# Optimization experiments

Hardware: AMD Instinct MI355X
Metric: run time of the kernel (lower is better)

## Reference

```python
import jax, jax.numpy as jnp
import numpy as np

D_MODEL = 256
D_FFN = 1024
N_HEADS = 8
N_LEVELS = 4
N_POINTS = 4
SPATIAL = np.array([[60, 100], [30, 50], [15, 25], [8, 13]], dtype=np.int32)  # (H, W) per level


def _layer_norm(x, g, b, eps=1e-5):
    mu = jnp.mean(x, axis=-1, keepdims=True)
    var = jnp.mean(jnp.square(x - mu), axis=-1, keepdims=True)
    return (x - mu) * jax.lax.rsqrt(var + eps) * g + b


def _bilinear_sample(v_l, loc, aw, H, W):
    # v_l: (B,H,W,h,hd); loc: (B,Lq,h,p,2) normalized [0,1]; aw: (B,Lq,h,p)
    B = v_l.shape[0]
    h = v_l.shape[3]
    x = loc[..., 0] * W - 0.5  # grid_sample align_corners=False convention
    y = loc[..., 1] * H - 0.5
    x0 = jnp.floor(x)
    y0 = jnp.floor(y)
    lx = x - x0
    ly = y - y0
    x0i = x0.astype(jnp.int32)
    y0i = y0.astype(jnp.int32)
    bi = jnp.arange(B)[:, None, None, None]
    hi = jnp.arange(h)[None, None, :, None]

    def g(xi, yi):
        valid = (xi >= 0) & (xi < W) & (yi >= 0) & (yi < H)
        xc = jnp.clip(xi, 0, W - 1)
        yc = jnp.clip(yi, 0, H - 1)
        return v_l[bi, yc, xc, hi] * valid[..., None].astype(v_l.dtype)  # zero padding

    w00 = (1 - lx) * (1 - ly)
    w01 = lx * (1 - ly)
    w10 = (1 - lx) * ly
    w11 = lx * ly
    samp = (g(x0i, y0i) * w00[..., None] + g(x0i + 1, y0i) * w01[..., None]
            + g(x0i, y0i + 1) * w10[..., None] + g(x0i + 1, y0i + 1) * w11[..., None])
    # weighted sum over sampling points -> (B,Lq,h,hd)
    return jnp.einsum('blhpd,blhp->blhd', samp, aw)


def _msda(q, val, ref, W_value, b_value, W_off, b_off, W_attn, b_attn, W_out, b_out):
    # mmcv MultiScaleDeformableAttention (batch_first, identity=query, eval-mode dropout)
    B, Lq, C = q.shape
    hd = C // N_HEADS
    v = (val @ W_value + b_value).reshape(B, -1, N_HEADS, hd)
    off = (q @ W_off + b_off).reshape(B, Lq, N_HEADS, N_LEVELS, N_POINTS, 2)
    aw = jax.nn.softmax((q @ W_attn + b_attn).reshape(B, Lq, N_HEADS, N_LEVELS * N_POINTS), axis=-1)
    aw = aw.reshape(B, Lq, N_HEADS, N_LEVELS, N_POINTS)
    normalizer = jnp.asarray(SPATIAL[:, ::-1].copy(), dtype=q.dtype)  # (levels, 2) = (W, H)
    loc = ref[:, :, None, :, None, :] + off / normalizer[None, None, None, :, None, :]
    out = jnp.zeros((B, Lq, N_HEADS, hd), q.dtype)
    start = 0
    for lvl in range(N_LEVELS):
        H, W = int(SPATIAL[lvl, 0]), int(SPATIAL[lvl, 1])
        v_l = v[:, start:start + H * W].reshape(B, H, W, N_HEADS, hd)
        start += H * W
        out = out + _bilinear_sample(v_l, loc[:, :, :, lvl], aw[:, :, :, lvl], H, W)
    return q + out.reshape(B, Lq, C) @ W_out + b_out  # identity + output_proj


def setup_inputs() -> dict:
    key = jax.random.key(0)
    ks = jax.random.split(key, 16)
    bs, cams, nq = 1, 6, 6400
    l = int(SPATIAL.prod(axis=1).sum())
    s = 0.02
    inp = {
        'query': jax.random.normal(ks[0], (bs, nq, D_MODEL), jnp.float32),
        'key': jax.random.normal(ks[1], (bs, cams, l, D_MODEL), jnp.float32),
        'value': jax.random.normal(ks[2], (bs, cams, l, D_MODEL), jnp.float32),
        'reference_points_cam': jax.random.uniform(ks[3], (cams, bs, nq, N_LEVELS, 2), jnp.float32),
        'spatial_shapes': jnp.asarray(SPATIAL),
        'level_start_index': jnp.asarray(np.concatenate([[0], np.cumsum(SPATIAL.prod(axis=1))[:-1]]).astype(np.int32)),
        'bev_mask': jax.random.randint(ks[4], (cams, bs, nq, 4), 0, 2).astype(jnp.int32),
        'W_value': jax.random.normal(ks[5], (D_MODEL, D_MODEL), jnp.float32) * s,
        'b_value': jnp.zeros((D_MODEL,), jnp.float32),
        'W_off': jax.random.normal(ks[6], (D_MODEL, N_HEADS * N_LEVELS * N_POINTS * 2), jnp.float32) * s,
        'b_off': jax.random.normal(ks[7], (N_HEADS * N_LEVELS * N_POINTS * 2,), jnp.float32) * s,
        'W_attn': jax.random.normal(ks[8], (D_MODEL, N_HEADS * N_LEVELS * N_POINTS), jnp.float32) * s,
        'b_attn': jnp.zeros((N_HEADS * N_LEVELS * N_POINTS,), jnp.float32),
        'W_out': jax.random.normal(ks[9], (D_MODEL, D_MODEL), jnp.float32) * s,
        'b_out': jnp.zeros((D_MODEL,), jnp.float32),
        'ln1_g': jnp.ones((D_MODEL,), jnp.float32),
        'ln1_b': jnp.zeros((D_MODEL,), jnp.float32),
        'W1': jax.random.normal(ks[10], (D_MODEL, D_FFN), jnp.float32) * s,
        'b1': jnp.zeros((D_FFN,), jnp.float32),
        'W2': jax.random.normal(ks[11], (D_FFN, D_MODEL), jnp.float32) * s,
        'b2': jnp.zeros((D_MODEL,), jnp.float32),
        'ln2_g': jnp.ones((D_MODEL,), jnp.float32),
        'ln2_b': jnp.zeros((D_MODEL,), jnp.float32),
    }
    return inp


def reference(query, key, value, reference_points_cam, spatial_shapes, level_start_index, bev_mask,
              W_value, b_value, W_off, b_off, W_attn, b_attn, W_out, b_out,
              ln1_g, ln1_b, W1, b1, W2, b2, ln2_g, ln2_b):
    bs, nq, C = query.shape
    cams = key.shape[1]
    l = key.shape[2]
    # per-camera query visibility taken from batch element 0 (as in original)
    cam_mask = (bev_mask[:, 0].sum(-1) > 0).astype(query.dtype)  # (cams, nq)
    # rebatch via masking: equivalent to gather-to-padded since attention is per-query
    q_rb = (query[:, None] * cam_mask[None, :, :, None]).reshape(bs * cams, nq, C)
    ref_rb = (jnp.transpose(reference_points_cam, (1, 0, 2, 3, 4))
              * cam_mask[None, :, :, None, None]).reshape(bs * cams, nq, N_LEVELS, 2)
    val = value.reshape(bs * cams, l, C)
    attn = _msda(q_rb, val, ref_rb, W_value, b_value, W_off, b_off, W_attn, b_attn, W_out, b_out)
    attn = attn.reshape(bs, cams, nq, C)
    # scatter-add back (only visible camera contributions)
    slots = jnp.einsum('bknc,kn->bnc', attn, cam_mask)
    # visibility count (full bev_mask, per batch element)
    count = (bev_mask.sum(-1) > 0).astype(query.dtype)  # (cams, bs, nq)
    count = jnp.maximum(count.transpose(1, 2, 0).sum(-1), 1.0)  # (bs, nq)
    slots = slots / count[..., None]
    x = _layer_norm(slots + query, ln1_g, ln1_b)
    ffn = jax.nn.relu(x @ W1 + b1) @ W2 + b2
    return _layer_norm(x + ffn, ln2_g, ln2_b)
```

## Files before the change

### kernel.cpp

```cpp
#include <hip/hip_runtime.h>
#include <math.h>

#define NQ      6400
#define NCAMS   6
#define LTOT    7979
#define DM      256
#define DFFN    1024

typedef __attribute__((ext_vector_type(8))) short bf16x8;
typedef __attribute__((ext_vector_type(4))) float f32x4;

__device__ inline unsigned short f32_to_bf16(float f) {
    unsigned u = __float_as_uint(f);
    unsigned r = u + 0x7FFF + ((u >> 16) & 1);
    return (unsigned short)(r >> 16);
}

__global__ __launch_bounds__(256) void cvt_kernel(
    const float* __restrict__ src, unsigned short* __restrict__ dst, int n8)
{
    int i = blockIdx.x * 256 + threadIdx.x;
    if (i >= n8) return;
    const float4* s = (const float4*)src + (size_t)i * 2;
    float4 a = s[0], b = s[1];
    uint4 o;
    o.x = f32_to_bf16(a.x) | ((unsigned)f32_to_bf16(a.y) << 16);
    o.y = f32_to_bf16(a.z) | ((unsigned)f32_to_bf16(a.w) << 16);
    o.z = f32_to_bf16(b.x) | ((unsigned)f32_to_bf16(b.y) << 16);
    o.w = f32_to_bf16(b.z) | ((unsigned)f32_to_bf16(b.w) << 16);
    *(uint4*)(dst + (size_t)i * 8) = o;
}

__global__ __launch_bounds__(256) void wt_kernel(
    const float* __restrict__ Wv, const float* __restrict__ Woff,
    const float* __restrict__ Wattn, const float* __restrict__ Wout,
    const float* __restrict__ W1, const float* __restrict__ W2,
    unsigned short* __restrict__ wsT)
{
    int b = blockIdx.x;
    const float* src; int K, N, t0, dstoff;
    if (b < 64)       { src = Wv;    K = 256;  N = 256;  t0 = 0;   dstoff = 0; }
    else if (b < 128) { src = Woff;  K = 256;  N = 256;  t0 = 64;  dstoff = 65536; }
    else if (b < 160) { src = Wattn; K = 256;  N = 128;  t0 = 128; dstoff = 131072; }
    else if (b < 224) { src = Wout;  K = 256;  N = 256;  t0 = 160; dstoff = 163840; }
    else if (b < 480) { src = W1;    K = 256;  N = 1024; t0 = 224; dstoff = 229376; }
    else              { src = W2;    K = 1024; N = 256;  t0 = 480; dstoff = 491520; }
    int t = b - t0;
    int ntn = N >> 5;
    int kt = t / ntn, nt = t - kt * ntn;
    __shared__ float tile[32][33];
    int tx = threadIdx.x & 31, ty = threadIdx.x >> 5;
    #pragma unroll
    for (int i = 0; i < 4; ++i)
        tile[ty + i * 8][tx] = src[(size_t)(kt * 32 + ty + i * 8) * N + nt * 32 + tx];
    __syncthreads();
    #pragma unroll
    for (int i = 0; i < 4; ++i) {
        int nn = nt * 32 + ty + i * 8;
        wsT[dstoff + (size_t)nn * K + kt * 32 + tx] = f32_to_bf16(tile[tx][ty + i * 8]);
    }
}

__global__ __launch_bounds__(256) void gemm_v_kernel(
    const unsigned short* __restrict__ A, const unsigned short* __restrict__ BT,
    const float* __restrict__ bias, unsigned short* __restrict__ Cb, int M)
{
    const int K = 256;
    __shared__ __align__(16) unsigned short As[128][40];
    __shared__ __align__(16) unsigned short Bs[128][40];

    const int tid  = threadIdx.x;
    const int wave = tid >> 6, lane = tid & 63;
    const int wm = wave >> 1, wn = wave & 1;
    const int quad = lane >> 4, l16 = lane & 15;
    const int m0 = blockIdx.y * 128, n0 = blockIdx.x * 128;

    f32x4 acc[4][4] = {};

    for (int k0 = 0; k0 < K; k0 += 32) {
        #pragma unroll
        for (int i = 0; i < 2; ++i) {
            int idx = tid + 256 * i;
            int r = idx >> 2, kc = (idx & 3) * 8;
            int gr = m0 + r;
            uint4 d = (gr < M) ? *(const uint4*)(A + (size_t)gr * K + k0 + kc)
                               : make_uint4(0u, 0u, 0u, 0u);
            uint2* dst = (uint2*)&As[r][kc];
            dst[0] = make_uint2(d.x, d.y);
            dst[1] = make_uint2(d.z, d.w);
        }
        #pragma unroll
        for (int i = 0; i < 2; ++i) {
            int idx = tid + 256 * i;
            int r = idx >> 2, kc = (idx & 3) * 8;
            uint4 d = *(const uint4*)(BT + (size_t)(n0 + r) * K + k0 + kc);
            uint2* dst = (uint2*)&Bs[r][kc];
            dst[0] = make_uint2(d.x, d.y);
            dst[1] = make_uint2(d.z, d.w);
        }
        __syncthreads();
        bf16x8 af[4], bfr[4];
        #pragma unroll
        for (int mi = 0; mi < 4; ++mi)
            af[mi] = *(const bf16x8*)&As[wm * 64 + mi * 16 + l16][quad * 8];
        #pragma unroll
        for (int ni = 0; ni < 4; ++ni)
            bfr[ni] = *(const bf16x8*)&Bs[wn * 64 + ni * 16 + l16][quad * 8];
        #pragma unroll
        for (int mi = 0; mi < 4; ++mi)
            #pragma unroll
            for (int ni = 0; ni < 4; ++ni)
                acc[mi][ni] = __builtin_amdgcn_mfma_f32_16x16x32_bf16(
                    af[mi], bfr[ni], acc[mi][ni], 0, 0, 0);
        __syncthreads();
    }

    #pragma unroll
    for (int mi = 0; mi < 4; ++mi) {
        #pragma unroll
        for (int r = 0; r < 4; ++r) {
            int gm = m0 + wm * 64 + mi * 16 + quad * 4 + r;
            if (gm >= M) continue;
            int cam = gm / LTOT;
            int pix = gm - cam * LTOT;
            #pragma unroll
            for (int ni = 0; ni < 4; ++ni) {
                int gn = n0 + wn * 64 + ni * 16 + l16;
                int head = gn >> 5, ch = gn & 31;
                float v = acc[mi][ni][r] + bias[gn];
                Cb[(((size_t)(cam * 8 + head)) * LTOT + pix) * 32 + ch] = f32_to_bf16(v);
            }
        }
    }
}

__global__ __launch_bounds__(256) void gemm64_kernel(
    const unsigned short* __restrict__ A, const unsigned short* __restrict__ BT,
    const float* __restrict__ bias, float* __restrict__ C,
    unsigned short* __restrict__ Cb,
    int M, int N, int K, int mode)
{
    __shared__ __align__(16) unsigned short As[64][40];
    __shared__ __align__(16) unsigned short Bs[128][40];

    const int tid  = threadIdx.x;
    const int wave = tid >> 6, lane = tid & 63;
    const int wm = wave >> 1, wn = wave & 1;
    const int quad = lane >> 4, l16 = lane & 15;
    const int m0 = blockIdx.y * 64, n0 = blockIdx.x * 128;

    f32x4 acc[2][4] = {};

    for (int k0 = 0; k0 < K; k0 += 32) {
        {
            int r = tid >> 2, kc = (tid & 3) * 8;
            int gr = m0 + r;
            uint4 d = (gr < M) ? *(const uint4*)(A + (size_t)gr * K + k0 + kc)
                               : make_uint4(0u, 0u, 0u, 0u);
            uint2* dst = (uint2*)&As[r][kc];
            dst[0] = make_uint2(d.x, d.y);
            dst[1] = make_uint2(d.z, d.w);
        }
        #pragma unroll
        for (int i = 0; i < 2; ++i) {
            int idx = tid + 256 * i;
            int r = idx >> 2, kc = (idx & 3) * 8;
            uint4 d = *(const uint4*)(BT + (size_t)(n0 + r) * K + k0 + kc);
            uint2* dst = (uint2*)&Bs[r][kc];
            dst[0] = make_uint2(d.x, d.y);
            dst[1] = make_uint2(d.z, d.w);
        }
        __syncthreads();
        bf16x8 af[2], bfr[4];
        #pragma unroll
        for (int mi = 0; mi < 2; ++mi)
            af[mi] = *(const bf16x8*)&As[wm * 32 + mi * 16 + l16][quad * 8];
        #pragma unroll
        for (int ni = 0; ni < 4; ++ni)
            bfr[ni] = *(const bf16x8*)&Bs[wn * 64 + ni * 16 + l16][quad * 8];
        #pragma unroll
        for (int mi = 0; mi < 2; ++mi)
            #pragma unroll
            for (int ni = 0; ni < 4; ++ni)
                acc[mi][ni] = __builtin_amdgcn_mfma_f32_16x16x32_bf16(
                    af[mi], bfr[ni], acc[mi][ni], 0, 0, 0);
        __syncthreads();
    }

    #pragma unroll
    for (int mi = 0; mi < 2; ++mi) {
        #pragma unroll
        for (int r = 0; r < 4; ++r) {
            int gm = m0 + wm * 32 + mi * 16 + quad * 4 + r;
            if (gm >= M) continue;
            #pragma unroll
            for (int ni = 0; ni < 4; ++ni) {
                int gn = n0 + wn * 64 + ni * 16 + l16;
                float v = acc[mi][ni][r] + (bias ? bias[gn] : 0.f);
                if (mode == 1) {
                    Cb[(size_t)gm * N + gn] = f32_to_bf16(fmaxf(v, 0.f));
                } else {
                    C[(size_t)gm * N + gn] = v;
                }
            }
        }
    }
}

__global__ __launch_bounds__(256) void qproj_kernel(
    const unsigned short* __restrict__ A, const unsigned short* __restrict__ WqT,
    const float* __restrict__ b_off, const float* __restrict__ b_attn,
    float* __restrict__ qoff, float* __restrict__ qaw)
{
    const int K = 256;
    __shared__ __align__(16) unsigned short As[64][40];
    __shared__ __align__(16) unsigned short Bs[128][40];

    const int tid  = threadIdx.x;
    const int wave = tid >> 6, lane = tid & 63;
    const int wm = wave >> 1, wn = wave & 1;
    const int quad = lane >> 4, l16 = lane & 15;
    const int m0 = blockIdx.y * 64, n0 = blockIdx.x * 128;
    const int is_attn = (n0 == 256);

    f32x4 acc[2][4] = {};

    for (int k0 = 0; k0 < K; k0 += 32) {
        {
            int r = tid >> 2, kc = (tid & 3) * 8;
            uint4 d = *(const uint4*)(A + (size_t)(m0 + r) * K + k0 + kc);
            uint2* dst = (uint2*)&As[r][kc];
            dst[0] = make_uint2(d.x, d.y);
            dst[1] = make_uint2(d.z, d.w);
        }
        #pragma unroll
        for (int i = 0; i < 2; ++i) {
            int idx = tid + 256 * i;
            int r = idx >> 2, kc = (idx & 3) * 8;
            uint4 d = *(const uint4*)(WqT + (size_t)(n0 + r) * K + k0 + kc);
            uint2* dst = (uint2*)&Bs[r][kc];
            dst[0] = make_uint2(d.x, d.y);
            dst[1] = make_uint2(d.z, d.w);
        }
        __syncthreads();
        bf16x8 af[2], bfr[4];
        #pragma unroll
        for (int mi = 0; mi < 2; ++mi)
            af[mi] = *(const bf16x8*)&As[wm * 32 + mi * 16 + l16][quad * 8];
        #pragma unroll
        for (int ni = 0; ni < 4; ++ni)
            bfr[ni] = *(const bf16x8*)&Bs[wn * 64 + ni * 16 + l16][quad * 8];
        #pragma unroll
        for (int mi = 0; mi < 2; ++mi)
            #pragma unroll
            for (int ni = 0; ni < 4; ++ni)
                acc[mi][ni] = __builtin_amdgcn_mfma_f32_16x16x32_bf16(
                    af[mi], bfr[ni], acc[mi][ni], 0, 0, 0);
        __syncthreads();
    }

    if (is_attn) {
        #pragma unroll
        for (int mi = 0; mi < 2; ++mi) {
            #pragma unroll
            for (int r = 0; r < 4; ++r) {
                int gm = m0 + wm * 32 + mi * 16 + quad * 4 + r;
                #pragma unroll
                for (int ni = 0; ni < 4; ++ni) {
                    int gn = wn * 64 + ni * 16 + l16;
                    float v = acc[mi][ni][r] + b_attn[gn];
                    float mx = v;
                    #pragma unroll
                    for (int s = 1; s < 16; s <<= 1)
                        mx = fmaxf(mx, __shfl_xor(mx, s, 64));
                    float e = __expf(v - mx);
                    float sum = e;
                    #pragma unroll
                    for (int s = 1; s < 16; s <<= 1)
                        sum += __shfl_xor(sum, s, 64);
                    qaw[(size_t)gm * 128 + gn] = e / sum;
                }
            }
        }
    } else {
        #pragma unroll
        for (int mi = 0; mi < 2; ++mi) {
            #pragma unroll
            for (int r = 0; r < 4; ++r) {
                int gm = m0 + wm * 32 + mi * 16 + quad * 4 + r;
                #pragma unroll
                for (int ni = 0; ni < 4; ++ni) {
                    int gn = n0 + wn * 64 + ni * 16 + l16;
                    qoff[(size_t)gm * 256 + gn] = acc[mi][ni][r] + b_off[gn];
                }
            }
        }
    }
}

__global__ __launch_bounds__(256) void sample_kernel(
    const unsigned short* __restrict__ vb,
    const float* __restrict__ qoff,
    const float* __restrict__ aw,
    const float* __restrict__ refpts,
    const int*   __restrict__ bev_mask,
    unsigned short* __restrict__ outsum,
    float* __restrict__ visb)
{
    const int bid = blockIdx.x;
    const int h   = bid & 7;
    const int q0  = (bid >> 3) * 16;
    const int tid = threadIdx.x;
    const int sq  = tid >> 4;
    const int tup = tid & 15;
    const int lvl = tup >> 2;
    const int n_s = q0 + sq;
    const int tg  = (tid >> 2) & 3;
    const int cg  = tid & 3;

    __shared__ int2  s_tab[4][272];
    __shared__ float s_vis[NCAMS][16];
    __shared__ int   s_cnt[NCAMS];
    __shared__ int   s_nvis[16];

    if (tid < 96) {
        int cam = tid >> 4, q = tid & 15;
        const int* bm = bev_mask + ((size_t)cam * NQ + q0 + q) * 4;
        s_vis[cam][q] = ((bm[0] + bm[1] + bm[2] + bm[3]) > 0) ? 1.f : 0.f;
    }
    __syncthreads();
    if (tid < NCAMS) {
        float s = 0.f;
        #pragma unroll
        for (int q = 0; q < 16; ++q) s += s_vis[tid][q];
        s_cnt[tid] = (int)s;
    }
    if (tid >= 32 && tid < 48) {
        int q = tid - 32;
        float s = 0.f;
        #pragma unroll
        for (int cam = 0; cam < NCAMS; ++cam) s += s_vis[cam][q];
        s_nvis[q] = (int)s;
    }
    __syncthreads();

    const float my_aw = aw[(size_t)n_s * 128 + h * 16 + tup];
    const float offx  = qoff[(size_t)n_s * 256 + h * 32 + tup * 2];
    const float offy  = qoff[(size_t)n_s * 256 + h * 32 + tup * 2 + 1];
    const int Wl   = (lvl == 0) ? 100 : (lvl == 1) ? 50 : (lvl == 2) ? 25 : 13;
    const int Hl   = (lvl == 0) ? 60  : (lvl == 1) ? 30 : (lvl == 2) ? 15 : 8;
    const int base = (lvl == 0) ? 0   : (lvl == 1) ? 6000 : (lvl == 2) ? 7500 : 7875;
    const float dx = offx / (float)Wl;
    const float dy = offy / (float)Hl;
    const int tabi = sq * 17 + tup;

    float a0 = 0.f, a1 = 0.f, a2 = 0.f, a3 = 0.f;
    float a4 = 0.f, a5 = 0.f, a6 = 0.f, a7 = 0.f;

    for (int k = 0; k < NCAMS; ++k) {
        if (s_cnt[k] == 0) continue;
        {
            const size_t rbase = (((size_t)k * NQ + n_s) * 4 + lvl) * 2;
            float fx = (refpts[rbase + 0] + dx) * (float)Wl - 0.5f;
            float fy = (refpts[rbase + 1] + dy) * (float)Hl - 0.5f;
            float x0f = floorf(fx), y0f = floorf(fy);
            float lx = fx - x0f, ly = fy - y0f;
            int x0 = (int)x0f, y0 = (int)y0f;
            int x1 = x0 + 1, y1 = y0 + 1;
            float wb = my_aw * s_vis[k][sq];
            float w00 = (1.f - lx) * (1.f - ly) * wb;
            float w01 = lx * (1.f - ly) * wb;
            float w10 = (1.f - lx) * ly * wb;
            float w11 = lx * ly * wb;
            bool vx0 = (x0 >= 0) & (x0 < Wl), vx1 = (x1 >= 0) & (x1 < Wl);
            bool vy0 = (y0 >= 0) & (y0 < Hl), vy1 = (y1 >= 0) & (y1 < Hl);
            s_tab[0][tabi] = make_int2((vx0 & vy0) ? (base + y0 * Wl + x0) * 64 : 0,
                                       __float_as_int((vx0 & vy0) ? w00 : 0.f));
            s_tab[1][tabi] = make_int2((vx1 & vy0) ? (base + y0 * Wl + x1) * 64 : 0,
                                       __float_as_int((vx1 & vy0) ? w01 : 0.f));
            s_tab[2][tabi] = make_int2((vx0 & vy1) ? (base + y1 * Wl + x0) * 64 : 0,
                                       __float_as_int((vx0 & vy1) ? w10 : 0.f));
            s_tab[3][tabi] = make_int2((vx1 & vy1) ? (base + y1 * Wl + x1) * 64 : 0,
                                       __float_as_int((vx1 & vy1) ? w11 : 0.f));
        }
        __syncthreads();
        const char* vkh = (const char*)vb + (size_t)(k * 8 + h) * (LTOT * 64) + cg * 16;
        #pragma unroll
        for (int j = 0; j < 4; ++j) {
            int ti = sq * 17 + tg * 4 + j;
            #pragma unroll
            for (int corner = 0; corner < 4; ++corner) {
                int2 t = s_tab[corner][ti];
                float w = __int_as_float(t.y);
                uint4 d = *(const uint4*)(vkh + t.x);
                a0 += w * __uint_as_float(d.x << 16);
                a1 += w * __uint_as_float(d.x & 0xFFFF0000u);
                a2 += w * __uint_as_float(d.y << 16);
                a3 += w * __uint_as_float(d.y & 0xFFFF0000u);
                a4 += w * __uint_as_float(d.z << 16);
                a5 += w * __uint_as_float(d.z & 0xFFFF0000u);
                a6 += w * __uint_as_float(d.w << 16);
                a7 += w * __uint_as_float(d.w & 0xFFFF0000u);
            }
        }
        __syncthreads();
    }

    a0 += __shfl_xor(a0, 4, 64); a0 += __shfl_xor(a0, 8, 64);
    a1 += __shfl_xor(a1, 4, 64); a1 += __shfl_xor(a1, 8, 64);
    a2 += __shfl_xor(a2, 4, 64); a2 += __shfl_xor(a2, 8, 64);
    a3 += __shfl_xor(a3, 4, 64); a3 += __shfl_xor(a3, 8, 64);
    a4 += __shfl_xor(a4, 4, 64); a4 += __shfl_xor(a4, 8, 64);
    a5 += __shfl_xor(a5, 4, 64); a5 += __shfl_xor(a5, 8, 64);
    a6 += __shfl_xor(a6, 4, 64); a6 += __shfl_xor(a6, 8, 64);
    a7 += __shfl_xor(a7, 4, 64); a7 += __shfl_xor(a7, 8, 64);

    if ((tid & 12) == 0) {
        int nv = s_nvis[sq];
        float sc = 1.f / (float)(nv > 0 ? nv : 1);
        uint4 o;
        o.x = f32_to_bf16(a0 * sc) | ((unsigned)f32_to_bf16(a1 * sc) << 16);
        o.y = f32_to_bf16(a2 * sc) | ((unsigned)f32_to_bf16(a3 * sc) << 16);
        o.z = f32_to_bf16(a4 * sc) | ((unsigned)f32_to_bf16(a5 * sc) << 16);
        o.w = f32_to_bf16(a6 * sc) | ((unsigned)f32_to_bf16(a7 * sc) << 16);
        *(uint4*)(outsum + (size_t)n_s * 256 + h * 32 + cg * 8) = o;
    }
    if (h == 0 && tid < 16) visb[q0 + tid] = (s_nvis[tid] > 0) ? 1.f : 0.f;
}

__device__ inline float block_sum_256(float v, float* red)
{
    #pragma unroll
    for (int o = 32; o > 0; o >>= 1) v += __shfl_down(v, o, 64);
    int lane = threadIdx.x & 63, w = threadIdx.x >> 6;
    if (lane == 0) red[w] = v;
    __syncthreads();
    float t = red[0] + red[1] + red[2] + red[3];
    __syncthreads();
    return t;
}

__global__ __launch_bounds__(256) void ln1_kernel(
    const float* __restrict__ gin, const float* __restrict__ query,
    const float* __restrict__ visb, const float* __restrict__ b_out,
    const float* __restrict__ g, const float* __restrict__ b,
    float* __restrict__ xout, unsigned short* __restrict__ xbf)
{
    __shared__ float red[4];
    int n = blockIdx.x, j = threadIdx.x;
    float vs = visb[n];
    size_t idx = (size_t)n * 256 + j;
    float t = gin[idx] + query[idx] * (1.f + vs) + vs * b_out[j];
    float mu = block_sum_256(t, red) * (1.f / 256.f);
    float d = t - mu;
    float var = block_sum_256(d * d, red) * (1.f / 256.f);
    float res = d * rsqrtf(var + 1e-5f) * g[j] + b[j];
    xout[idx] = res;
    xbf[idx] = f32_to_bf16(res);
}

__global__ __launch_bounds__(256) void ln2_kernel(
    const float* __restrict__ x, const float* __restrict__ ffn,
    const float* __restrict__ g, const float* __restrict__ b,
    float* __restrict__ out)
{
    __shared__ float red[4];
    int n = blockIdx.x, j = threadIdx.x;
    size_t idx = (size_t)n * 256 + j;
    float t = x[idx] + ffn[idx];
    float mu = block_sum_256(t, red) * (1.f / 256.f);
    float d = t - mu;
    float var = block_sum_256(d * d, red) * (1.f / 256.f);
    out[idx] = d * rsqrtf(var + 1e-5f) * g[j] + b[j];
}

extern "C" void kernel_launch(void* const* d_in, const int* in_sizes, int n_in,
                              void* d_out, int out_size, void* d_ws, size_t ws_size,
                              hipStream_t stream)
{
    const float* query   = (const float*)d_in[0];
    const float* value   = (const float*)d_in[2];
    const float* refpts  = (const float*)d_in[3];
    const int*   bevmask = (const int*)d_in[6];
    const float* W_value = (const float*)d_in[7];
    const float* b_value = (const float*)d_in[8];
    const float* W_off   = (const float*)d_in[9];
    const float* b_off   = (const float*)d_in[10];
    const float* W_attn  = (const float*)d_in[11];
    const float* b_attn  = (const float*)d_in[12];
    const float* W_out   = (const float*)d_in[13];
    const float* b_out   = (const float*)d_in[14];
    const float* ln1_g   = (const float*)d_in[15];
    const float* ln1_b   = (const float*)d_in[16];
    const float* W1      = (const float*)d_in[17];
    const float* b1      = (const float*)d_in[18];
    const float* W2      = (const float*)d_in[19];
    const float* b2      = (const float*)d_in[20];
    const float* ln2_g   = (const float*)d_in[21];
    const float* ln2_b   = (const float*)d_in[22];
    float* out = (float*)d_out;

    char* ws = (char*)d_ws;
    unsigned short* vb       = (unsigned short*)(ws + 0);
    float*          xbuf     = (float*)(ws + 0);
    float*          ln_in    = (float*)(ws + 7000000);
    unsigned short* xbf      = (unsigned short*)(ws + 14000000);
    unsigned short* value_bf = (unsigned short*)(ws + 24600000);
    float*          qoff     = (float*)(ws + 24600000);
    float*          qaw      = (float*)(ws + 31200000);
    unsigned short* outsum   = (unsigned short*)(ws + 34500000);
    unsigned short* hbf      = (unsigned short*)(ws + 37800000);
    unsigned short* query_bf = (unsigned short*)(ws + 51000000);
    float*          ffnout   = (float*)(ws + 54300000);
    float*          visb     = (float*)(ws + 60900000);
    unsigned short* wsT      = (unsigned short*)(ws + 61000000);

    unsigned short* WvT = wsT;
    unsigned short* WqT = wsT + 65536;
    unsigned short* WoT = wsT + 163840;
    unsigned short* W1T = wsT + 229376;
    unsigned short* W2T = wsT + 491520;

    const int MV = NCAMS * LTOT;

    cvt_kernel<<<dim3((MV * 256 / 8 + 255) / 256), 256, 0, stream>>>(
        value, value_bf, MV * 256 / 8);
    cvt_kernel<<<dim3((NQ * 256 / 8 + 255) / 256), 256, 0, stream>>>(
        query, query_bf, NQ * 256 / 8);
    wt_kernel<<<dim3(736), 256, 0, stream>>>(
        W_value, W_off, W_attn, W_out, W1, W2, wsT);
    gemm_v_kernel<<<dim3(2, (MV + 127) / 128), 256, 0, stream>>>(
        value_bf, WvT, b_value, vb, MV);
    qproj_kernel<<<dim3(3, 100), 256, 0, stream>>>(
        query_bf, WqT, b_off, b_attn, qoff, qaw);
    sample_kernel<<<dim3(3200), 256, 0, stream>>>(
        vb, qoff, qaw, refpts, bevmask, outsum, visb);
    gemm64_kernel<<<dim3(2, 100), 256, 0, stream>>>(
        outsum, WoT, nullptr, ln_in, nullptr, NQ, 256, 256, 0);
    ln1_kernel<<<dim3(NQ), 256, 0, stream>>>(
        ln_in, query, visb, b_out, ln1_g, ln1_b, xbuf, xbf);
    gemm64_kernel<<<dim3(8, 100), 256, 0, stream>>>(
        xbf, W1T, b1, nullptr, hbf, NQ, DFFN, 256, 1);
    gemm64_kernel<<<dim3(2, 100), 256, 0, stream>>>(
        hbf, W2T, b2, ffnout, nullptr, NQ, 256, DFFN, 0);
    ln2_kernel<<<dim3(NQ), 256, 0, stream>>>(
        xbuf, ffnout, ln2_g, ln2_b, out);
}
```

Measured before the change: 332.2 us.

## Fuse bf16 conversion into GEMMs, fuse out-proj with LN1, split-K FFN2, double-buffer sampling

```diff
diff --git a/kernel.cpp b/kernel.cpp
--- a/kernel.cpp
+++ b/kernel.cpp
@@ -14,21 +14,6 @@
     unsigned u = __float_as_uint(f);
     unsigned r = u + 0x7FFF + ((u >> 16) & 1);
     return (unsigned short)(r >> 16);
-}
-
-__global__ __launch_bounds__(256) void cvt_kernel(
-    const float* __restrict__ src, unsigned short* __restrict__ dst, int n8)
-{
-    int i = blockIdx.x * 256 + threadIdx.x;
-    if (i >= n8) return;
-    const float4* s = (const float4*)src + (size_t)i * 2;
-    float4 a = s[0], b = s[1];
-    uint4 o;
-    o.x = f32_to_bf16(a.x) | ((unsigned)f32_to_bf16(a.y) << 16);
-    o.y = f32_to_bf16(a.z) | ((unsigned)f32_to_bf16(a.w) << 16);
-    o.z = f32_to_bf16(b.x) | ((unsigned)f32_to_bf16(b.y) << 16);
-    o.w = f32_to_bf16(b.z) | ((unsigned)f32_to_bf16(b.w) << 16);
-    *(uint4*)(dst + (size_t)i * 8) = o;
 }
 
 __global__ __launch_bounds__(256) void wt_kernel(
@@ -62,7 +47,7 @@
 }
 
 __global__ __launch_bounds__(256) void gemm_v_kernel(
-    const unsigned short* __restrict__ A, const unsigned short* __restrict__ BT,
+    const float* __restrict__ A, const unsigned short* __restrict__ BT,
     const float* __restrict__ bias, unsigned short* __restrict__ Cb, int M)
 {
     const int K = 256;
@@ -83,20 +68,23 @@
             int idx = tid + 256 * i;
             int r = idx >> 2, kc = (idx & 3) * 8;
             int gr = m0 + r;
-            uint4 d = (gr < M) ? *(const uint4*)(A + (size_t)gr * K + k0 + kc)
-                               : make_uint4(0u, 0u, 0u, 0u);
-            uint2* dst = (uint2*)&As[r][kc];
-            dst[0] = make_uint2(d.x, d.y);
-            dst[1] = make_uint2(d.z, d.w);
+            float4 f0, f1;
+            if (gr < M) {
+                f0 = *(const float4*)(A + (size_t)gr * K + k0 + kc);
+                f1 = *(const float4*)(A + (size_t)gr * K + k0 + kc + 4);
+            } else { f0 = make_float4(0,0,0,0); f1 = f0; }
+            uint4 o;
+            o.x = f32_to_bf16(f0.x) | ((unsigned)f32_to_bf16(f0.y) << 16);
+            o.y = f32_to_bf16(f0.z) | ((unsigned)f32_to_bf16(f0.w) << 16);
+            o.z = f32_to_bf16(f1.x) | ((unsigned)f32_to_bf16(f1.y) << 16);
+            o.w = f32_to_bf16(f1.z) | ((unsigned)f32_to_bf16(f1.w) << 16);
+            *(uint4*)&As[r][kc] = o;
         }
         #pragma unroll
         for (int i = 0; i < 2; ++i) {
             int idx = tid + 256 * i;
             int r = idx >> 2, kc = (idx & 3) * 8;
-            uint4 d = *(const uint4*)(BT + (size_t)(n0 + r) * K + k0 + kc);
-            uint2* dst = (uint2*)&Bs[r][kc];
-            dst[0] = make_uint2(d.x, d.y);
-            dst[1] = make_uint2(d.z, d.w);
+            *(uint4*)&Bs[r][kc] = *(const uint4*)(BT + (size_t)(n0 + r) * K + k0 + kc);
         }
         __syncthreads();
         bf16x8 af[4], bfr[4];
@@ -134,81 +122,8 @@
     }
 }
 
-__global__ __launch_bounds__(256) void gemm64_kernel(
-    const unsigned short* __restrict__ A, const unsigned short* __restrict__ BT,
-    const float* __restrict__ bias, float* __restrict__ C,
-    unsigned short* __restrict__ Cb,
-    int M, int N, int K, int mode)
-{
-    __shared__ __align__(16) unsigned short As[64][40];
-    __shared__ __align__(16) unsigned short Bs[128][40];
-
-    const int tid  = threadIdx.x;
-    const int wave = tid >> 6, lane = tid & 63;
-    const int wm = wave >> 1, wn = wave & 1;
-    const int quad = lane >> 4, l16 = lane & 15;
-    const int m0 = blockIdx.y * 64, n0 = blockIdx.x * 128;
-
-    f32x4 acc[2][4] = {};
-
-    for (int k0 = 0; k0 < K; k0 += 32) {
-        {
-            int r = tid >> 2, kc = (tid & 3) * 8;
-            int gr = m0 + r;
-            uint4 d = (gr < M) ? *(const uint4*)(A + (size_t)gr * K + k0 + kc)
-                               : make_uint4(0u, 0u, 0u, 0u);
-            uint2* dst = (uint2*)&As[r][kc];
-            dst[0] = make_uint2(d.x, d.y);
-            dst[1] = make_uint2(d.z, d.w);
-        }
-        #pragma unroll
-        for (int i = 0; i < 2; ++i) {
-            int idx = tid + 256 * i;
-            int r = idx >> 2, kc = (idx & 3) * 8;
-            uint4 d = *(const uint4*)(BT + (size_t)(n0 + r) * K + k0 + kc);
-            uint2* dst = (uint2*)&Bs[r][kc];
-            dst[0] = make_uint2(d.x, d.y);
-            dst[1] = make_uint2(d.z, d.w);
-        }
-        __syncthreads();
-        bf16x8 af[2], bfr[4];
-        #pragma unroll
-        for (int mi = 0; mi < 2; ++mi)
-            af[mi] = *(const bf16x8*)&As[wm * 32 + mi * 16 + l16][quad * 8];
-        #pragma unroll
-        for (int ni = 0; ni < 4; ++ni)
-            bfr[ni] = *(const bf16x8*)&Bs[wn * 64 + ni * 16 + l16][quad * 8];
-        #pragma unroll
-        for (int mi = 0; mi < 2; ++mi)
-            #pragma unroll
-            for (int ni = 0; ni < 4; ++ni)
-                acc[mi][ni] = __builtin_amdgcn_mfma_f32_16x16x32_bf16(
-                    af[mi], bfr[ni], acc[mi][ni], 0, 0, 0);
-        __syncthreads();
-    }
-
-    #pragma unroll
-    for (int mi = 0; mi < 2; ++mi) {
-        #pragma unroll
-        for (int r = 0; r < 4; ++r) {
-            int gm = m0 + wm * 32 + mi * 16 + quad * 4 + r;
-            if (gm >= M) continue;
-            #pragma unroll
-            for (int ni = 0; ni < 4; ++ni) {
-                int gn = n0 + wn * 64 + ni * 16 + l16;
-                float v = acc[mi][ni][r] + (bias ? bias[gn] : 0.f);
-                if (mode == 1) {
-                    Cb[(size_t)gm * N + gn] = f32_to_bf16(fmaxf(v, 0.f));
-                } else {
-                    C[(size_t)gm * N + gn] = v;
-                }
-            }
-        }
-    }
-}
-
 __global__ __launch_bounds__(256) void qproj_kernel(
-    const unsigned short* __restrict__ A, const unsigned short* __restrict__ WqT,
+    const float* __restrict__ A, const unsigned short* __restrict__ WqT,
     const float* __restrict__ b_off, const float* __restrict__ b_attn,
     float* __restrict__ qoff, float* __restrict__ qaw)
 {
@@ -228,19 +143,20 @@
     for (int k0 = 0; k0 < K; k0 += 32) {
         {
             int r = tid >> 2, kc = (tid & 3) * 8;
-            uint4 d = *(const uint4*)(A + (size_t)(m0 + r) * K + k0 + kc);
-            uint2* dst = (uint2*)&As[r][kc];
-            dst[0] = make_uint2(d.x, d.y);
-            dst[1] = make_uint2(d.z, d.w);
+            float4 f0 = *(const float4*)(A + (size_t)(m0 + r) * K + k0 + kc);
+            float4 f1 = *(const float4*)(A + (size_t)(m0 + r) * K + k0 + kc + 4);
+            uint4 o;
+            o.x = f32_to_bf16(f0.x) | ((unsigned)f32_to_bf16(f0.y) << 16);
+            o.y = f32_to_bf16(f0.z) | ((unsigned)f32_to_bf16(f0.w) << 16);
+            o.z = f32_to_bf16(f1.x) | ((unsigned)f32_to_bf16(f1.y) << 16);
+            o.w = f32_to_bf16(f1.z) | ((unsigned)f32_to_bf16(f1.w) << 16);
+            *(uint4*)&As[r][kc] = o;
         }
         #pragma unroll
         for (int i = 0; i < 2; ++i) {
             int idx = tid + 256 * i;
             int r = idx >> 2, kc = (idx & 3) * 8;
-            uint4 d = *(const uint4*)(WqT + (size_t)(n0 + r) * K + k0 + kc);
-            uint2* dst = (uint2*)&Bs[r][kc];
-            dst[0] = make_uint2(d.x, d.y);
-            dst[1] = make_uint2(d.z, d.w);
+            *(uint4*)&Bs[r][kc] = *(const uint4*)(WqT + (size_t)(n0 + r) * K + k0 + kc);
         }
         __syncthreads();
         bf16x8 af[2], bfr[4];
@@ -318,7 +234,7 @@
     const int tg  = (tid >> 2) & 3;
     const int cg  = tid & 3;
 
-    __shared__ int2  s_tab[4][272];
+    __shared__ int2  s_tab[2][4][272];
     __shared__ float s_vis[NCAMS][16];
     __shared__ int   s_cnt[NCAMS];
     __shared__ int   s_nvis[16];
@@ -354,43 +270,53 @@
     const float dy = offy / (float)Hl;
     const int tabi = sq * 17 + tup;
 
+    int vcams[NCAMS], nvc = 0;
+    #pragma unroll
+    for (int k = 0; k < NCAMS; ++k)
+        if (s_cnt[k] > 0) vcams[nvc++] = k;
+
+    auto build_tab = [&](int k, int buf) {
+        const size_t rbase = (((size_t)k * NQ + n_s) * 4 + lvl) * 2;
+        float fx = (refpts[rbase + 0] + dx) * (float)Wl - 0.5f;
+        float fy = (refpts[rbase + 1] + dy) * (float)Hl - 0.5f;
+        float x0f = floorf(fx), y0f = floorf(fy);
+        float lx = fx - x0f, ly = fy - y0f;
+        int x0 = (int)x0f, y0 = (int)y0f;
+        int x1 = x0 + 1, y1 = y0 + 1;
+        float wb = my_aw * s_vis[k][sq];
+        float w00 = (1.f - lx) * (1.f - ly) * wb;
+        float w01 = lx * (1.f - ly) * wb;
+        float w10 = (1.f - lx) * ly * wb;
+        float w11 = lx * ly * wb;
+        bool vx0 = (x0 >= 0) & (x0 < Wl), vx1 = (x1 >= 0) & (x1 < Wl);
+        bool vy0 = (y0 >= 0) & (y0 < Hl), vy1 = (y1 >= 0) & (y1 < Hl);
+        s_tab[buf][0][tabi] = make_int2((vx0 & vy0) ? (base + y0 * Wl + x0) * 64 : 0,
+                                        __float_as_int((vx0 & vy0) ? w00 : 0.f));
+        s_tab[buf][1][tabi] = make_int2((vx1 & vy0) ? (base + y0 * Wl + x1) * 64 : 0,
+                                        __float_as_int((vx1 & vy0) ? w01 : 0.f));
+        s_tab[buf][2][tabi] = make_int2((vx0 & vy1) ? (base + y1 * Wl + x0) * 64 : 0,
+                                        __float_as_int((vx0 & vy1) ? w10 : 0.f));
+        s_tab[buf][3][tabi] = make_int2((vx1 & vy1) ? (base + y1 * Wl + x1) * 64 : 0,
+                                        __float_as_int((vx1 & vy1) ? w11 : 0.f));
+    };
+
     float a0 = 0.f, a1 = 0.f, a2 = 0.f, a3 = 0.f;
     float a4 = 0.f, a5 = 0.f, a6 = 0.f, a7 = 0.f;
 
-    for (int k = 0; k < NCAMS; ++k) {
-        if (s_cnt[k] == 0) continue;
-        {
-            const size_t rbase = (((size_t)k * NQ + n_s) * 4 + lvl) * 2;
-            float fx = (refpts[rbase + 0] + dx) * (float)Wl - 0.5f;
-            float fy = (refpts[rbase + 1] + dy) * (float)Hl - 0.5f;
-            float x0f = floorf(fx), y0f = floorf(fy);
-            float lx = fx - x0f, ly = fy - y0f;
-            int x0 = (int)x0f, y0 = (int)y0f;
-            int x1 = x0 + 1, y1 = y0 + 1;
-            float wb = my_aw * s_vis[k][sq];
-            float w00 = (1.f - lx) * (1.f - ly) * wb;
-            float w01 = lx * (1.f - ly) * wb;
-            float w10 = (1.f - lx) * ly * wb;
-            float w11 = lx * ly * wb;
-            bool vx0 = (x0 >= 0) & (x0 < Wl), vx1 = (x1 >= 0) & (x1 < Wl);
-            bool vy0 = (y0 >= 0) & (y0 < Hl), vy1 = (y1 >= 0) & (y1 < Hl);
-            s_tab[0][tabi] = make_int2((vx0 & vy0) ? (base + y0 * Wl + x0) * 64 : 0,
-                                       __float_as_int((vx0 & vy0) ? w00 : 0.f));
-            s_tab[1][tabi] = make_int2((vx1 & vy0) ? (base + y0 * Wl + x1) * 64 : 0,
-                                       __float_as_int((vx1 & vy0) ? w01 : 0.f));
-            s_tab[2][tabi] = make_int2((vx0 & vy1) ? (base + y1 * Wl + x0) * 64 : 0,
-                                       __float_as_int((vx0 & vy1) ? w10 : 0.f));
-            s_tab[3][tabi] = make_int2((vx1 & vy1) ? (base + y1 * Wl + x1) * 64 : 0,
-                                       __float_as_int((vx1 & vy1) ? w11 : 0.f));
-        }
-        __syncthreads();
+    if (nvc > 0) build_tab(vcams[0], 0);
+    __syncthreads();
+
+    int pb = 0;
+    for (int i = 0; i < nvc; ++i) {
+        int k = vcams[i];
+        if (i + 1 < nvc) build_tab(vcams[i + 1], pb ^ 1);
         const char* vkh = (const char*)vb + (size_t)(k * 8 + h) * (LTOT * 64) + cg * 16;
         #pragma unroll
         for (int j = 0; j < 4; ++j) {
             int ti = sq * 17 + tg * 4 + j;
             #pragma unroll
             for (int corner = 0; corner < 4; ++corner) {
-                int2 t = s_tab[corner][ti];
+                int2 t = s_tab[pb][corner][ti];
                 float w = __int_as_float(t.y);
                 uint4 d = *(const uint4*)(vkh + t.x);
                 a0 += w * __uint_as_float(d.x << 16);
@@ -404,6 +330,7 @@
             }
         }
         __syncthreads();
+        pb ^= 1;
     }
 
     a0 += __shfl_xor(a0, 4, 64); a0 += __shfl_xor(a0, 8, 64);
@@ -428,6 +355,179 @@
     if (h == 0 && tid < 16) visb[q0 + tid] = (s_nvis[tid] > 0) ? 1.f : 0.f;
 }
 
+__global__ __launch_bounds__(256) void projln1_kernel(
+    const unsigned short* __restrict__ A, const unsigned short* __restrict__ BT,
+    const float* __restrict__ query, const float* __restrict__ visb,
+    const float* __restrict__ b_out, const float* __restrict__ g,
+    const float* __restrict__ b,
+    float* __restrict__ xout, unsigned short* __restrict__ xbf)
+{
+    const int K = 256;
+    __shared__ __align__(16) unsigned short As[32][40];
+    __shared__ __align__(16) unsigned short Bs[256][40];
+    __shared__ float sred[2][4][4][2];
+    __shared__ float ssred[2][4][4][2];
+    __shared__ float s_mu[32], s_rs[32];
+
+    const int tid  = threadIdx.x;
+    const int wave = tid >> 6, lane = tid & 63;
+    const int wm = wave >> 1, wn = wave & 1;
+    const int quad = lane >> 4, l16 = lane & 15;
+    const int m0 = blockIdx.x * 32;
+
+    f32x4 acc[8] = {};
+
+    for (int k0 = 0; k0 < K; k0 += 32) {
+        {
+            int r = tid >> 3, kc = (tid & 7) * 4;
+            *(uint2*)&As[r][kc] = *(const uint2*)(A + (size_t)(m0 + r) * K + k0 + kc);
+        }
+        {
+            const unsigned short* src = BT + (size_t)tid * K + k0;
+            uint4 d0 = *(const uint4*)(src);
+            uint4 d1 = *(const uint4*)(src + 8);
+            uint4 d2 = *(const uint4*)(src + 16);
+            uint4 d3 = *(const uint4*)(src + 24);
+            *(uint4*)&Bs[tid][0]  = d0;
+            *(uint4*)&Bs[tid][8]  = d1;
+            *(uint4*)&Bs[tid][16] = d2;
+            *(uint4*)&Bs[tid][24] = d3;
+        }
+        __syncthreads();
+        bf16x8 af = *(const bf16x8*)&As[wm * 16 + l16][quad * 8];
+        #pragma unroll
+        for (int ni = 0; ni < 8; ++ni) {
+            bf16x8 bfr = *(const bf16x8*)&Bs[wn * 128 + ni * 16 + l16][quad * 8];
+            acc[ni] = __builtin_amdgcn_mfma_f32_16x16x32_bf16(af, bfr, acc[ni], 0, 0, 0);
+        }
+        __syncthreads();
+    }
+
+    float vals[8][4];
+    #pragma unroll
+    for (int r = 0; r < 4; ++r) {
+        int gm = m0 + wm * 16 + quad * 4 + r;
+        float vs = visb[gm];
+        float s = 0.f, ss = 0.f;
+        #pragma unroll
+        for (int ni = 0; ni < 8; ++ni) {
+            int gn = wn * 128 + ni * 16 + l16;
+            float v = acc[ni][r] + vs * b_out[gn]
+                    + query[(size_t)gm * 256 + gn] * (1.f + vs);
+            vals[ni][r] = v;
+            s += v; ss += v * v;
+        }
+        #pragma unroll
+        for (int m = 1; m < 16; m <<= 1) {
+            s  += __shfl_xor(s,  m, 64);
+            ss += __shfl_xor(ss, m, 64);
+        }
+        if (l16 == 0) {
+            sred[wm][quad][r][wn]  = s;
+            ssred[wm][quad][r][wn] = ss;
+        }
+    }
+    __syncthreads();
+    if (tid < 32) {
+        int lwm = tid >> 4, lq = (tid >> 2) & 3, lr = tid & 3;
+        float s  = sred[lwm][lq][lr][0]  + sred[lwm][lq][lr][1];
+        float ss = ssred[lwm][lq][lr][0] + ssred[lwm][lq][lr][1];
+        float mu = s * (1.f / 256.f);
+        float var = ss * (1.f / 256.f) - mu * mu;
+        s_mu[tid] = mu;
+        s_rs[tid] = rsqrtf(var + 1e-5f);
+    }
+    __syncthreads();
+
+    #pragma unroll
+    for (int r = 0; r < 4; ++r) {
+        int rowl = wm * 16 + quad * 4 + r;
+        int gm = m0 + rowl;
+        float mu = s_mu[rowl], rs = s_rs[rowl];
+        #pragma unroll
+        for (int ni = 0; ni < 8; ++ni) {
+            int gn = wn * 128 + ni * 16 + l16;
+            float res = (vals[ni][r] - mu) * rs * g[gn] + b[gn];
+            xout[(size_t)gm * 256 + gn] = res;
+            xbf[(size_t)gm * 256 + gn] = f32_to_bf16(res);
+        }
+    }
+}
+
+__global__ __launch_bounds__(256) void gemm64_kernel(
+    const unsigned short* __restrict__ A, const unsigned short* __restrict__ BT,
+    const float* __restrict__ bias, float* __restrict__ C,
+    unsigned short* __restrict__ Cb,
+    int M, int N, int K, int mode)
+{
+    __shared__ __align__(16) unsigned short As[64][40];
+    __shared__ __align__(16) unsigned short Bs[128][40];
+
+    const int tid  = threadIdx.x;
+    const int wave = tid >> 6, lane = tid & 63;
+    const int wm = wave >> 1, wn = wave & 1;
+    const int quad = lane >> 4, l16 = lane & 15;
+    const int m0 = blockIdx.y * 64, n0 = blockIdx.x * 128;
+    const int nz = gridDim.z;
+    const int klen = K / nz;
+    const int kbase = blockIdx.z * klen;
+
+    f32x4 acc[2][4] = {};
+
+    for (int k0 = kbase; k0 < kbase + klen; k0 += 32) {
+        {
+            int r = tid >> 2, kc = (tid & 3) * 8;
+            int gr = m0 + r;
+            uint4 d = (gr < M) ? *(const uint4*)(A + (size_t)gr * K + k0 + kc)
+                               : make_uint4(0u, 0u, 0u, 0u);
+            *(uint4*)&As[r][kc] = d;
+        }
+        #pragma unroll
+        for (int i = 0; i < 2; ++i) {
+            int idx = tid + 256 * i;
+            int r = idx >> 2, kc = (idx & 3) * 8;
+            *(uint4*)&Bs[r][kc] = *(const uint4*)(BT + (size_t)(n0 + r) * K + k0 + kc);
+        }
+        __syncthreads();
+        bf16x8 af[2], bfr[4];
+        #pragma unroll
+        for (int mi = 0; mi < 2; ++mi)
+            af[mi] = *(const bf16x8*)&As[wm * 32 + mi * 16 + l16][quad * 8];
+        #pragma unroll
+        for (int ni = 0; ni < 4; ++ni)
+            bfr[ni] = *(const bf16x8*)&Bs[wn * 64 + ni * 16 + l16][quad * 8];
+        #pragma unroll
+        for (int mi = 0; mi < 2; ++mi)
+            #pragma unroll
+            for (int ni = 0; ni < 4; ++ni)
+                acc[mi][ni] = __builtin_amdgcn_mfma_f32_16x16x32_bf16(
+                    af[mi], bfr[ni], acc[mi][ni], 0, 0, 0);
+        __syncthreads();
+    }
+
+    const float* bz = (blockIdx.z == 0) ? bias : nullptr;
+    float* Cz = C ? (C + (size_t)blockIdx.z * M * N) : nullptr;
+
+    #pragma unroll
+    for (int mi = 0; mi < 2; ++mi) {
+        #pragma unroll
+        for (int r = 0; r < 4; ++r) {
+            int gm = m0 + wm * 32 + mi * 16 + quad * 4 + r;
+            if (gm >= M) continue;
+            #pragma unroll
+            for (int ni = 0; ni < 4; ++ni) {
+                int gn = n0 + wn * 64 + ni * 16 + l16;
+                float v = acc[mi][ni][r] + (bz ? bz[gn] : 0.f);
+                if (mode == 1) {
+                    Cb[(size_t)gm * N + gn] = f32_to_bf16(fmaxf(v, 0.f));
+                } else {
+                    Cz[(size_t)gm * N + gn] = v;
+                }
+            }
+        }
+    }
+}
+
 __device__ inline float block_sum_256(float v, float* red)
 {
     #pragma unroll
@@ -440,34 +540,16 @@
     return t;
 }
 
-__global__ __launch_bounds__(256) void ln1_kernel(
-    const float* __restrict__ gin, const float* __restrict__ query,
-    const float* __restrict__ visb, const float* __restrict__ b_out,
-    const float* __restrict__ g, const float* __restrict__ b,
-    float* __restrict__ xout, unsigned short* __restrict__ xbf)
-{
-    __shared__ float red[4];
-    int n = blockIdx.x, j = threadIdx.x;
-    float vs = visb[n];
-    size_t idx = (size_t)n * 256 + j;
-    float t = gin[idx] + query[idx] * (1.f + vs) + vs * b_out[j];
-    float mu = block_sum_256(t, red) * (1.f / 256.f);
-    float d = t - mu;
-    float var = block_sum_256(d * d, red) * (1.f / 256.f);
-    float res = d * rsqrtf(var + 1e-5f) * g[j] + b[j];
-    xout[idx] = res;
-    xbf[idx] = f32_to_bf16(res);
-}
-
 __global__ __launch_bounds__(256) void ln2_kernel(
-    const float* __restrict__ x, const float* __restrict__ ffn,
+    const float* __restrict__ x, const float* __restrict__ f0,
+    const float* __restrict__ f1,
     const float* __restrict__ g, const float* __restrict__ b,
     float* __restrict__ out)
 {
     __shared__ float red[4];
     int n = blockIdx.x, j = threadIdx.x;
     size_t idx = (size_t)n * 256 + j;
-    float t = x[idx] + ffn[idx];
+    float t = x[idx] + f0[idx] + f1[idx];
     float mu = block_sum_256(t, red) * (1.f / 256.f);
     float d = t - mu;
     float var = block_sum_256(d * d, red) * (1.f / 256.f);
@@ -501,19 +583,16 @@
     float* out = (float*)d_out;
 
     char* ws = (char*)d_ws;
-    unsigned short* vb       = (unsigned short*)(ws + 0);
-    float*          xbuf     = (float*)(ws + 0);
-    float*          ln_in    = (float*)(ws + 7000000);
-    unsigned short* xbf      = (unsigned short*)(ws + 14000000);
-    unsigned short* value_bf = (unsigned short*)(ws + 24600000);
-    float*          qoff     = (float*)(ws + 24600000);
-    float*          qaw      = (float*)(ws + 31200000);
-    unsigned short* outsum   = (unsigned short*)(ws + 34500000);
-    unsigned short* hbf      = (unsigned short*)(ws + 37800000);
-    unsigned short* query_bf = (unsigned short*)(ws + 51000000);
-    float*          ffnout   = (float*)(ws + 54300000);
-    float*          visb     = (float*)(ws + 60900000);
-    unsigned short* wsT      = (unsigned short*)(ws + 61000000);
+    unsigned short* vb     = (unsigned short*)(ws + 0);
+    float*          xbuf   = (float*)(ws + 0);
+    unsigned short* xbf    = (unsigned short*)(ws + 7000000);
+    unsigned short* hbf    = (unsigned short*)(ws + 11000000);
+    float*          qoff   = (float*)(ws + 25000000);
+    float*          qaw    = (float*)(ws + 32000000);
+    unsigned short* outsum = (unsigned short*)(ws + 35300000);
+    float*          visb   = (float*)(ws + 38600000);
+    unsigned short* wsT    = (unsigned short*)(ws + 38700000);
+    float*          ffnout = (float*)(ws + 41000000);
 
     unsigned short* WvT = wsT;
     unsigned short* WqT = wsT + 65536;
@@ -523,26 +602,20 @@
 
     const int MV = NCAMS * LTOT;
 
-    cvt_kernel<<<dim3((MV * 256 / 8 + 255) / 256), 256, 0, stream>>>(
-        value, value_bf, MV * 256 / 8);
-    cvt_kernel<<<dim3((NQ * 256 / 8 + 255) / 256), 256, 0, stream>>>(
-        query, query_bf, NQ * 256 / 8);
     wt_kernel<<<dim3(736), 256, 0, stream>>>(
         W_value, W_off, W_attn, W_out, W1, W2, wsT);
     gemm_v_kernel<<<dim3(2, (MV + 127) / 128), 256, 0, stream>>>(
-        value_bf, WvT, b_value, vb, MV);
+        value, WvT, b_value, vb, MV);
     qproj_kernel<<<dim3(3, 100), 256, 0, stream>>>(
-        query_bf, WqT, b_off, b_attn, qoff, qaw);
+        query, WqT, b_off, b_attn, qoff, qaw);
     sample_kernel<<<dim3(3200), 256, 0, stream>>>(
         vb, qoff, qaw, refpts, bevmask, outsum, visb);
-    gemm64_kernel<<<dim3(2, 100), 256, 0, stream>>>(
-        outsum, WoT, nullptr, ln_in, nullptr, NQ, 256, 256, 0);
-    ln1_kernel<<<dim3(NQ), 256, 0, stream>>>(
-        ln_in, query, visb, b_out, ln1_g, ln1_b, xbuf, xbf);
-    gemm64_kernel<<<dim3(8, 100), 256, 0, stream>>>(
+    projln1_kernel<<<dim3(200), 256, 0, stream>>>(
+        outsum, WoT, query, visb, b_out, ln1_g, ln1_b, xbuf, xbf);
+    gemm64_kernel<<<dim3(8, 100, 1), 256, 0, stream>>>(
         xbf, W1T, b1, nullptr, hbf, NQ, DFFN, 256, 1);
-    gemm64_kernel<<<dim3(2, 100), 256, 0, stream>>>(
+    gemm64_kernel<<<dim3(2, 100, 2), 256, 0, stream>>>(
         hbf, W2T, b2, ffnout, nullptr, NQ, 256, DFFN, 0);
     ln2_kernel<<<dim3(NQ), 256, 0, stream>>>(
-        xbuf, ffnout, ln2_g, ln2_b, out);
-}
+        xbuf, ffnout, ffnout + (size_t)NQ * 256, ln2_g, ln2_b, out);
+}
```

After: 321.7 us. -3.1%, faster.
